# Performance work log

Hardware: AMD Instinct MI355X
Metric: run time of the kernel (lower is better)

## Reference

```python
import jax, jax.numpy as jnp
import numpy as np

N_NODES = 8192
DIM = 512

def setup_inputs() -> dict:
    key = jax.random.key(0)
    k1, k2, k3, k4 = jax.random.split(key, 4)
    x = jax.random.normal(k1, (N_NODES, DIM), dtype=jnp.float32)
    adj = jax.random.uniform(k2, (N_NODES, N_NODES), dtype=jnp.float32)
    # nn.Linear(dim, dim): weight [out, in], bias [out]
    bound = 1.0 / np.sqrt(DIM)
    W = jax.random.uniform(k3, (DIM, DIM), minval=-bound, maxval=bound, dtype=jnp.float32)
    b = jax.random.uniform(k4, (DIM,), minval=-bound, maxval=bound, dtype=jnp.float32)
    return {"x": x, "adj": adj, "W": W, "b": b}

def reference(x, adj, W, b):
    # agg = adj @ x : [N, dim]
    agg = jnp.matmul(adj, x)
    # Linear: agg @ W.T + b, then ReLU
    out = jnp.matmul(agg, W.T) + b
    return jax.nn.relu(out)
```

## Files before the change

kernel.cpp:

```cpp
#include <hip/hip_runtime.h>

typedef __bf16 bf16_t;
typedef bf16_t bf16x8 __attribute__((ext_vector_type(8)));
typedef bf16_t bf16x4 __attribute__((ext_vector_type(4)));
typedef float f32x4 __attribute__((ext_vector_type(4)));

#define N_NODES 8192
#define DIM 512

__global__ __launch_bounds__(256) void k_transpose_x(const float* __restrict__ x,
                                                     bf16_t* __restrict__ xT) {
  __shared__ float tile[64][65];
  const int m0 = blockIdx.x * 64;
  const int n0 = blockIdx.y * 64;
  const int t = threadIdx.x;
  const int r = t >> 4;
  const int c = (t & 15) << 2;
#pragma unroll
  for (int i = 0; i < 4; ++i) {
    f32x4 v = *(const f32x4*)&x[(size_t)(m0 + r + i * 16) * DIM + n0 + c];
    tile[r + i * 16][c + 0] = v.x;
    tile[r + i * 16][c + 1] = v.y;
    tile[r + i * 16][c + 2] = v.z;
    tile[r + i * 16][c + 3] = v.w;
  }
  __syncthreads();
#pragma unroll
  for (int i = 0; i < 4; ++i) {
    const int rn = r + i * 16;
    bf16x4 o = {(bf16_t)tile[c + 0][rn], (bf16_t)tile[c + 1][rn],
                (bf16_t)tile[c + 2][rn], (bf16_t)tile[c + 3][rn]};
    *(bf16x4*)&xT[(size_t)(n0 + rn) * N_NODES + m0 + c] = o;
  }
}

__global__ __launch_bounds__(256) void k_cvt_w(const float* __restrict__ W,
                                               bf16_t* __restrict__ Wb) {
  const int t = blockIdx.x * 256 + threadIdx.x;
  f32x4 v = *(const f32x4*)&W[(size_t)t * 4];
  bf16x4 o = {(bf16_t)v.x, (bf16_t)v.y, (bf16_t)v.z, (bf16_t)v.w};
  *(bf16x4*)&Wb[(size_t)t * 4] = o;
}

template <bool A_F32, bool EPI_BIAS_RELU>
__global__ __launch_bounds__(256, 2) void k_gemm(const void* __restrict__ Av,
                                                 const bf16_t* __restrict__ B,
                                                 const float* __restrict__ bias,
                                                 void* __restrict__ Cv, int K) {
  constexpr int LDA = 72;
  constexpr int LDB = 72;
  __shared__ bf16_t As[64 * LDA];
  __shared__ bf16_t Bs[128 * LDB];

  const int b = blockIdx.x;
  const int j8 = b & 7;
  const int kb = b >> 3;
  const int n_tile = kb & 3;
  const int m_tile = (kb >> 2) * 8 + j8;
  const int m0 = m_tile * 64;
  const int n0 = n_tile * 128;

  const int t = threadIdx.x;
  const int lane = t & 63;
  const int w = t >> 6;
  const int wr = w & 1;
  const int wc = w >> 1;
  const int lrow = lane & 15;
  const int quad = lane >> 4;

  const int ar = t >> 2, aq = t & 3;
  const int br = t >> 1, bq = t & 1;

  const float* apf = (const float*)Av + (size_t)(m0 + ar) * K + aq * 16;
  const bf16_t* apb = (const bf16_t*)Av + (size_t)(m0 + ar) * K + aq * 16;
  const bf16_t* bp = B + (size_t)(n0 + br) * K + bq * 32;
  bf16_t* aw = &As[ar * LDA + aq * 16];
  bf16_t* bw = &Bs[br * LDB + bq * 32];

  f32x4 apre[4];
  bf16x8 apreb[2];
  bf16x8 bpre[4];

  auto load_pre = [&](int k0) {
    if constexpr (A_F32) {
#pragma unroll
      for (int i = 0; i < 4; ++i) apre[i] = *(const f32x4*)(apf + k0 + i * 4);
    } else {
#pragma unroll
      for (int i = 0; i < 2; ++i) apreb[i] = *(const bf16x8*)(apb + k0 + i * 8);
    }
#pragma unroll
    for (int i = 0; i < 4; ++i) bpre[i] = *(const bf16x8*)(bp + k0 + i * 8);
  };

  load_pre(0);
  f32x4 acc[2][4] = {};

  for (int k0 = 0; k0 < K; k0 += 64) {
    bf16x8 a0{}, a1{};
    if constexpr (A_F32) {
#pragma unroll
      for (int i = 0; i < 4; ++i) {
        a0[i] = (bf16_t)apre[0][i];
        a0[i + 4] = (bf16_t)apre[1][i];
        a1[i] = (bf16_t)apre[2][i];
        a1[i + 4] = (bf16_t)apre[3][i];
      }
    } else {
      a0 = apreb[0];
      a1 = apreb[1];
    }
    bf16x8 b0 = bpre[0], b1 = bpre[1], b2 = bpre[2], b3 = bpre[3];
    __syncthreads();
    *(bf16x8*)aw = a0;
    *(bf16x8*)(aw + 8) = a1;
    *(bf16x8*)bw = b0;
    *(bf16x8*)(bw + 8) = b1;
    *(bf16x8*)(bw + 16) = b2;
    *(bf16x8*)(bw + 24) = b3;
    __syncthreads();
    if (k0 + 64 < K) load_pre(k0 + 64);
#pragma unroll
    for (int kk = 0; kk < 64; kk += 32) {
      bf16x8 af0 = *(const bf16x8*)&As[(wr * 32 + 0 + lrow) * LDA + kk + quad * 8];
      bf16x8 af1 = *(const bf16x8*)&As[(wr * 32 + 16 + lrow) * LDA + kk + quad * 8];
      bf16x8 bf0 = *(const bf16x8*)&Bs[(wc * 64 + 0 + lrow) * LDB + kk + quad * 8];
      bf16x8 bf1 = *(const bf16x8*)&Bs[(wc * 64 + 16 + lrow) * LDB + kk + quad * 8];
      bf16x8 bf2 = *(const bf16x8*)&Bs[(wc * 64 + 32 + lrow) * LDB + kk + quad * 8];
      bf16x8 bf3 = *(const bf16x8*)&Bs[(wc * 64 + 48 + lrow) * LDB + kk + quad * 8];
      acc[0][0] = __builtin_amdgcn_mfma_f32_16x16x32_bf16(af0, bf0, acc[0][0], 0, 0, 0);
      acc[0][1] = __builtin_amdgcn_mfma_f32_16x16x32_bf16(af0, bf1, acc[0][1], 0, 0, 0);
      acc[0][2] = __builtin_amdgcn_mfma_f32_16x16x32_bf16(af0, bf2, acc[0][2], 0, 0, 0);
      acc[0][3] = __builtin_amdgcn_mfma_f32_16x16x32_bf16(af0, bf3, acc[0][3], 0, 0, 0);
      acc[1][0] = __builtin_amdgcn_mfma_f32_16x16x32_bf16(af1, bf0, acc[1][0], 0, 0, 0);
      acc[1][1] = __builtin_amdgcn_mfma_f32_16x16x32_bf16(af1, bf1, acc[1][1], 0, 0, 0);
      acc[1][2] = __builtin_amdgcn_mfma_f32_16x16x32_bf16(af1, bf2, acc[1][2], 0, 0, 0);
      acc[1][3] = __builtin_amdgcn_mfma_f32_16x16x32_bf16(af1, bf3, acc[1][3], 0, 0, 0);
    }
  }

#pragma unroll
  for (int i = 0; i < 2; ++i)
#pragma unroll
    for (int j = 0; j < 4; ++j) {
      const int col = n0 + wc * 64 + j * 16 + lrow;
      float bj = 0.0f;
      if constexpr (EPI_BIAS_RELU) bj = bias[col];
#pragma unroll
      for (int r = 0; r < 4; ++r) {
        const int row = m0 + wr * 32 + i * 16 + quad * 4 + r;
        if constexpr (EPI_BIAS_RELU) {
          float v = acc[i][j][r] + bj;
          ((float*)Cv)[(size_t)row * DIM + col] = v > 0.0f ? v : 0.0f;
        } else {
          ((bf16_t*)Cv)[(size_t)row * DIM + col] = (bf16_t)acc[i][j][r];
        }
      }
    }
}

extern "C" void kernel_launch(void* const* d_in, const int* in_sizes, int n_in,
                              void* d_out, int out_size, void* d_ws, size_t ws_size,
                              hipStream_t stream) {
  const float* x = (const float*)d_in[0];
  const float* adj = (const float*)d_in[1];
  const float* W = (const float*)d_in[2];
  const float* b = (const float*)d_in[3];
  float* out = (float*)d_out;

  bf16_t* xT = (bf16_t*)d_ws;
  bf16_t* Wb = xT + (size_t)DIM * N_NODES;
  bf16_t* agg = Wb + (size_t)DIM * DIM;

  k_transpose_x<<<dim3(N_NODES / 64, DIM / 64), 256, 0, stream>>>(x, xT);
  k_cvt_w<<<dim3((DIM * DIM / 4) / 256), 256, 0, stream>>>(W, Wb);
  k_gemm<true, false><<<dim3(512), 256, 0, stream>>>((const void*)adj, xT, nullptr,
                                                     (void*)agg, N_NODES);
  k_gemm<false, true><<<dim3(512), 256, 0, stream>>>((const void*)agg, Wb, b,
                                                     (void*)out, DIM);
}
```

Baseline: 517.4 us.

## Split-K the adjacency GEMM with larger double-buffered tiles and fused partial reduction

The big adj@x GEMM moves to 128x128 tiles with 512 threads, LDS double buffering and register prefetch two steps ahead. K is split four ways into fp32 partial slabs when workspace allows. The second GEMM sums the partials while loading its A operand, then applies bias and ReLU. This raises block count and data reuse for the memory-bound first GEMM, at the cost of writing and reading extra fp32 partial buffers.

```diff
diff --git a/kernel.cpp b/kernel.cpp
--- a/kernel.cpp
+++ b/kernel.cpp
@@ -42,22 +42,24 @@
   *(bf16x4*)&Wb[(size_t)t * 4] = o;
 }
 
-template <bool A_F32, bool EPI_BIAS_RELU>
-__global__ __launch_bounds__(256, 2) void k_gemm(const void* __restrict__ Av,
-                                                 const bf16_t* __restrict__ B,
-                                                 const float* __restrict__ bias,
-                                                 void* __restrict__ Cv, int K) {
-  constexpr int LDA = 72;
-  constexpr int LDB = 72;
-  __shared__ bf16_t As[64 * LDA];
-  __shared__ bf16_t Bs[128 * LDB];
+template <int S>
+__global__ __launch_bounds__(512, 4) void k_gemm1(const float* __restrict__ A,
+                                                  const bf16_t* __restrict__ Bt,
+                                                  float* __restrict__ P) {
+  constexpr int K = N_NODES;
+  constexpr int KC = K / S;
+  constexpr int NIT = KC / 32;
+  constexpr int LD = 40;
+  __shared__ bf16_t As[2][128 * LD];
+  __shared__ bf16_t Bs[2][128 * LD];
 
   const int b = blockIdx.x;
-  const int j8 = b & 7;
-  const int kb = b >> 3;
-  const int n_tile = kb & 3;
-  const int m_tile = (kb >> 2) * 8 + j8;
-  const int m0 = m_tile * 64;
+  const int xcd = b & 7;
+  const int i6 = b >> 3;
+  const int n_tile = i6 & 3;
+  const int s = (i6 >> 2) & (S - 1);
+  const int mg = (i6 >> 2) / S;
+  const int m0 = (mg * 8 + xcd) * 128;
   const int n0 = n_tile * 128;
 
   const int t = threadIdx.x;
@@ -67,50 +69,124 @@
   const int wc = w >> 1;
   const int lrow = lane & 15;
   const int quad = lane >> 4;
-
+  const int sr = t >> 2;
+  const int sq = t & 3;
+
+  const float* ap = A + (size_t)(m0 + sr) * K + s * KC + sq * 8;
+  const bf16_t* bp = Bt + (size_t)(n0 + sr) * K + s * KC + sq * 8;
+  const int wofs = sr * LD + sq * 8;
+
+  f32x4 pa0[2], pa1[2];
+  bf16x8 pb[2];
+  auto load_pre = [&](int k0, int sl) {
+    pa0[sl] = *(const f32x4*)(ap + k0);
+    pa1[sl] = *(const f32x4*)(ap + k0 + 4);
+    pb[sl] = *(const bf16x8*)(bp + k0);
+  };
+  auto stage = [&](int sl, int buf) {
+    bf16x8 av;
+#pragma unroll
+    for (int z = 0; z < 4; ++z) {
+      av[z] = (bf16_t)pa0[sl][z];
+      av[z + 4] = (bf16_t)pa1[sl][z];
+    }
+    *(bf16x8*)&As[buf][wofs] = av;
+    *(bf16x8*)&Bs[buf][wofs] = pb[sl];
+  };
+
+  load_pre(0, 0);
+  stage(0, 0);
+  if (NIT > 1) load_pre(32, 1);
+  f32x4 acc[4][2] = {};
+  __syncthreads();
+
+  int cur = 0;
+#pragma unroll 2
+  for (int it = 0; it < NIT; ++it) {
+    if (it + 2 < NIT) load_pre((it + 2) * 32, it & 1);
+    bf16x8 af[4], bfr[2];
+#pragma unroll
+    for (int ii = 0; ii < 4; ++ii)
+      af[ii] = *(const bf16x8*)&As[cur][(wr * 64 + ii * 16 + lrow) * LD + quad * 8];
+#pragma unroll
+    for (int jj = 0; jj < 2; ++jj)
+      bfr[jj] = *(const bf16x8*)&Bs[cur][(wc * 32 + jj * 16 + lrow) * LD + quad * 8];
+#pragma unroll
+    for (int ii = 0; ii < 4; ++ii)
+#pragma unroll
+      for (int jj = 0; jj < 2; ++jj)
+        acc[ii][jj] = __builtin_amdgcn_mfma_f32_16x16x32_bf16(af[ii], bfr[jj], acc[ii][jj], 0, 0, 0);
+    if (it + 1 < NIT) stage((it + 1) & 1, cur ^ 1);
+    __syncthreads();
+    cur ^= 1;
+  }
+
+  float* Pp = P + (size_t)s * N_NODES * DIM;
+#pragma unroll
+  for (int ii = 0; ii < 4; ++ii)
+#pragma unroll
+    for (int jj = 0; jj < 2; ++jj) {
+      const int col = n0 + wc * 32 + jj * 16 + lrow;
+#pragma unroll
+      for (int r = 0; r < 4; ++r) {
+        const int row = m0 + wr * 64 + ii * 16 + quad * 4 + r;
+        Pp[(size_t)row * DIM + col] = acc[ii][jj][r];
+      }
+    }
+}
+
+template <int S>
+__global__ __launch_bounds__(256, 2) void k_gemm2(const float* __restrict__ P,
+                                                  const bf16_t* __restrict__ Bw,
+                                                  const float* __restrict__ bias,
+                                                  float* __restrict__ out) {
+  constexpr int K = DIM;
+  constexpr int LDA = 72;
+  constexpr int LDB = 72;
+  constexpr size_t PS = (size_t)N_NODES * DIM;
+  __shared__ bf16_t As[64 * LDA];
+  __shared__ bf16_t Bs[128 * LDB];
+
+  const int b = blockIdx.x;
+  const int n0 = (b & 3) * 128;
+  const int m0 = (b >> 2) * 64;
+  const int t = threadIdx.x;
+  const int lane = t & 63;
+  const int w = t >> 6;
+  const int wr = w & 1;
+  const int wc = w >> 1;
+  const int lrow = lane & 15;
+  const int quad = lane >> 4;
   const int ar = t >> 2, aq = t & 3;
   const int br = t >> 1, bq = t & 1;
 
-  const float* apf = (const float*)Av + (size_t)(m0 + ar) * K + aq * 16;
-  const bf16_t* apb = (const bf16_t*)Av + (size_t)(m0 + ar) * K + aq * 16;
-  const bf16_t* bp = B + (size_t)(n0 + br) * K + bq * 32;
+  const float* ap = P + (size_t)(m0 + ar) * K + aq * 16;
+  const bf16_t* bp = Bw + (size_t)(n0 + br) * K + bq * 32;
   bf16_t* aw = &As[ar * LDA + aq * 16];
   bf16_t* bw = &Bs[br * LDB + bq * 32];
 
-  f32x4 apre[4];
-  bf16x8 apreb[2];
-  bf16x8 bpre[4];
-
-  auto load_pre = [&](int k0) {
-    if constexpr (A_F32) {
-#pragma unroll
-      for (int i = 0; i < 4; ++i) apre[i] = *(const f32x4*)(apf + k0 + i * 4);
-    } else {
-#pragma unroll
-      for (int i = 0; i < 2; ++i) apreb[i] = *(const bf16x8*)(apb + k0 + i * 8);
-    }
-#pragma unroll
-    for (int i = 0; i < 4; ++i) bpre[i] = *(const bf16x8*)(bp + k0 + i * 8);
-  };
-
-  load_pre(0);
   f32x4 acc[2][4] = {};
 
   for (int k0 = 0; k0 < K; k0 += 64) {
-    bf16x8 a0{}, a1{};
-    if constexpr (A_F32) {
-#pragma unroll
-      for (int i = 0; i < 4; ++i) {
-        a0[i] = (bf16_t)apre[0][i];
-        a0[i + 4] = (bf16_t)apre[1][i];
-        a1[i] = (bf16_t)apre[2][i];
-        a1[i + 4] = (bf16_t)apre[3][i];
-      }
-    } else {
-      a0 = apreb[0];
-      a1 = apreb[1];
-    }
-    bf16x8 b0 = bpre[0], b1 = bpre[1], b2 = bpre[2], b3 = bpre[3];
+    f32x4 av[4];
+#pragma unroll
+    for (int z = 0; z < 4; ++z) av[z] = *(const f32x4*)(ap + k0 + z * 4);
+#pragma unroll
+    for (int s2 = 1; s2 < S; ++s2)
+#pragma unroll
+      for (int z = 0; z < 4; ++z) av[z] += *(const f32x4*)(ap + s2 * PS + k0 + z * 4);
+    bf16x8 b0 = *(const bf16x8*)(bp + k0);
+    bf16x8 b1 = *(const bf16x8*)(bp + k0 + 8);
+    bf16x8 b2 = *(const bf16x8*)(bp + k0 + 16);
+    bf16x8 b3 = *(const bf16x8*)(bp + k0 + 24);
+    bf16x8 a0, a1;
+#pragma unroll
+    for (int z = 0; z < 4; ++z) {
+      a0[z] = (bf16_t)av[0][z];
+      a0[z + 4] = (bf16_t)av[1][z];
+      a1[z] = (bf16_t)av[2][z];
+      a1[z + 4] = (bf16_t)av[3][z];
+    }
     __syncthreads();
     *(bf16x8*)aw = a0;
     *(bf16x8*)(aw + 8) = a1;
@@ -119,7 +195,6 @@
     *(bf16x8*)(bw + 16) = b2;
     *(bf16x8*)(bw + 24) = b3;
     __syncthreads();
-    if (k0 + 64 < K) load_pre(k0 + 64);
 #pragma unroll
     for (int kk = 0; kk < 64; kk += 32) {
       bf16x8 af0 = *(const bf16x8*)&As[(wr * 32 + 0 + lrow) * LDA + kk + quad * 8];
@@ -144,17 +219,12 @@
 #pragma unroll
     for (int j = 0; j < 4; ++j) {
       const int col = n0 + wc * 64 + j * 16 + lrow;
-      float bj = 0.0f;
-      if constexpr (EPI_BIAS_RELU) bj = bias[col];
+      const float bj = bias[col];
 #pragma unroll
       for (int r = 0; r < 4; ++r) {
         const int row = m0 + wr * 32 + i * 16 + quad * 4 + r;
-        if constexpr (EPI_BIAS_RELU) {
-          float v = acc[i][j][r] + bj;
-          ((float*)Cv)[(size_t)row * DIM + col] = v > 0.0f ? v : 0.0f;
-        } else {
-          ((bf16_t*)Cv)[(size_t)row * DIM + col] = (bf16_t)acc[i][j][r];
-        }
+        float v = acc[i][j][r] + bj;
+        out[(size_t)row * DIM + col] = v > 0.0f ? v : 0.0f;
       }
     }
 }
@@ -170,12 +240,18 @@
 
   bf16_t* xT = (bf16_t*)d_ws;
   bf16_t* Wb = xT + (size_t)DIM * N_NODES;
-  bf16_t* agg = Wb + (size_t)DIM * DIM;
+  float* P = (float*)(Wb + (size_t)DIM * DIM);
+  const size_t base = (size_t)DIM * N_NODES * 2 + (size_t)DIM * DIM * 2;
+  const size_t pslab = (size_t)N_NODES * DIM * 4;
 
   k_transpose_x<<<dim3(N_NODES / 64, DIM / 64), 256, 0, stream>>>(x, xT);
   k_cvt_w<<<dim3((DIM * DIM / 4) / 256), 256, 0, stream>>>(W, Wb);
-  k_gemm<true, false><<<dim3(512), 256, 0, stream>>>((const void*)adj, xT, nullptr,
-                                                     (void*)agg, N_NODES);
-  k_gemm<false, true><<<dim3(512), 256, 0, stream>>>((const void*)agg, Wb, b,
-                                                     (void*)out, DIM);
-}
+
+  if (ws_size >= base + 4 * pslab) {
+    k_gemm1<4><<<dim3(256 * 4), 512, 0, stream>>>(adj, xT, P);
+    k_gemm2<4><<<dim3(512), 256, 0, stream>>>(P, Wb, b, out);
+  } else {
+    k_gemm1<1><<<dim3(256), 512, 0, stream>>>(adj, xT, P);
+    k_gemm2<1><<<dim3(512), 256, 0, stream>>>(P, Wb, b, out);
+  }
+}
```

Result: no change. 508.1 us (-1.8%).
